# Kernel tuning notes

Measured on AMD Instinct MI355X. Metric: run time of the kernel, lower is better.

Reference implementation:

```python
import jax, jax.numpy as jnp
import numpy as np

TAU = 2.0        # LIF membrane time constant
VTH = 0.5        # spike threshold
EPS = 1e-5       # BatchNorm eps
ALPHA = 2.0      # ATan surrogate alpha (spikingjelly default)


@jax.custom_vjp
def atan_heaviside(x):
    # forward: Heaviside spike; backward: ATan surrogate gradient
    return (x >= 0.0).astype(x.dtype)

def _ah_fwd(x):
    return atan_heaviside(x), x

def _ah_bwd(x, g):
    return (g * (ALPHA / 2.0) / (1.0 + (jnp.pi / 2.0 * ALPHA * x) ** 2),)

atan_heaviside.defvjp(_ah_fwd, _ah_bwd)


def lif_multistep(x):
    # x: [T, ...] -> spikes [T, ...]; hard reset to 0, decay_input=True
    def step(v, xt):
        v = v + (xt - v) / TAU
        s = atan_heaviside(v - VTH)
        v = v * (1.0 - jax.lax.stop_gradient(s))  # detach_reset=True
        return v, s
    v0 = jnp.zeros_like(x[0])
    _, spikes = jax.lax.scan(step, v0, x)
    return spikes


def tape_pe(d_model, max_len, dtype):
    # tAPE (ConvTran): sinusoidal PE with d_model/max_len frequency scaling
    pos = jnp.arange(max_len, dtype=dtype)[:, None]
    div = jnp.exp(jnp.arange(0, d_model, 2, dtype=dtype) * (-np.log(10000.0) / d_model))
    arg = pos * div * (d_model / max_len)
    pe = jnp.zeros((max_len, d_model), dtype)
    pe = pe.at[:, 0::2].set(jnp.sin(arg))
    pe = pe.at[:, 1::2].set(jnp.cos(arg))
    return pe  # [N, D]


def setup_inputs() -> dict:
    key = jax.random.key(0)
    k1, k2 = jax.random.split(key)
    T, B, N, P, D = 4, 64, 196, 768, 256
    x = jax.random.normal(k1, (T, B, N, P), dtype=jnp.float32)
    W = jax.random.normal(k2, (D, P), dtype=jnp.float32) * 0.02
    gamma = jnp.ones((D,), dtype=jnp.float32)
    beta = jnp.zeros((D,), dtype=jnp.float32)
    return {"x": x, "W": W, "gamma": gamma, "beta": beta}


def reference(x, W, gamma, beta):
    T, B, N, P = x.shape
    D = W.shape[0]
    # patch linear (no bias): [T,B,N,P] @ [D,P]^T -> [T,B,N,D]
    h = jnp.einsum('tbnp,dp->tbnd', x, W)
    h = jnp.transpose(h, (0, 1, 3, 2))  # [T,B,D,N]
    # BatchNorm1d over channel D (training-mode batch stats over T*B and N)
    mean = h.mean(axis=(0, 1, 3), keepdims=True)
    var = ((h - mean) ** 2).mean(axis=(0, 1, 3), keepdims=True)
    h = (h - mean) * jax.lax.rsqrt(var + EPS)
    h = h * gamma[None, None, :, None] + beta[None, None, :, None]
    # LIF spiking neuron scan over T
    h = lif_multistep(h)
    # tAPE positional encoding (broadcast [D,N] over T,B) + second LIF
    h = h + tape_pe(D, N, h.dtype).T
    h = lif_multistep(h)
    return jnp.transpose(h, (0, 1, 3, 2))  # [T,B,N,D]
```

## Files before the change

kernel.cpp:

```cpp
#include <hip/hip_runtime.h>
#include <cmath>

#define T_    4
#define B_    64
#define N_    196
#define P_    768
#define D_    256
#define BN_   (B_*N_)
#define M_    (T_*BN_)
#define SITES (BN_*D_)

#define TILE  64
#define TK    16
#define MBLKS (M_/TILE)
#define NBLKS (D_/TILE)
#define LSTR  70

typedef __attribute__((ext_vector_type(2))) float f32x2;

extern "C" __global__ __launch_bounds__(256)
void gemm_f32emu(const float* __restrict__ x, const float* __restrict__ w,
                 float* __restrict__ h) {
#pragma clang fp contract(off)
    __shared__ __align__(16) f32x2 As2[TK/2][LSTR];
    __shared__ __align__(16) f32x2 Bs2[TK/2][LSTR];

    const int tid  = threadIdx.x;
    const int tx   = tid & 15;
    const int ty   = tid >> 4;
    const int bid  = blockIdx.x;
    const int xcd  = bid & 7;
    const int lin  = bid >> 3;
    const int m0   = (xcd * 98 + (lin >> 2)) * TILE;
    const int d0   = (lin & 3) * TILE;
    const int lrow = tid >> 2;
    const int kq   = tid & 3;
    const int lk   = kq * 4;
    const int srow  = lrow + 2 * ((lrow >> 4) & 3);
    const int abase = ty * 4 + 2 * ((ty >> 2) & 3);
    const int bbase = tx * 4 + 2 * ((tx >> 2) & 3);

    f32x2 acc[4][4][2];
#pragma unroll
    for (int i = 0; i < 4; ++i)
#pragma unroll
        for (int j = 0; j < 4; ++j)
#pragma unroll
            for (int p = 0; p < 2; ++p) acc[i][j][p] = f32x2{0.0f, 0.0f};

    for (int k0 = 0; k0 < P_; k0 += TK) {
        const float4 av = *(const float4*)(x + (size_t)(m0 + lrow) * P_ + k0 + lk);
        const float4 bv = *(const float4*)(w + (size_t)(d0 + lrow) * P_ + k0 + lk);
        As2[kq * 2 + 0][srow] = f32x2{av.x, av.y};
        As2[kq * 2 + 1][srow] = f32x2{av.z, av.w};
        Bs2[kq * 2 + 0][srow] = f32x2{bv.x, bv.y};
        Bs2[kq * 2 + 1][srow] = f32x2{bv.z, bv.w};
        __syncthreads();
#pragma unroll
        for (int kp = 0; kp < TK / 2; ++kp) {
            const int pi = kp & 1;
            const f32x2* Ar = As2[kp];
            const f32x2* Br = Bs2[kp];
            f32x2 a2[4], b2[4];
#pragma unroll
            for (int i = 0; i < 4; ++i) a2[i] = Ar[abase + i];
#pragma unroll
            for (int j = 0; j < 4; ++j) b2[j] = Br[bbase + j];
#pragma unroll
            for (int i = 0; i < 4; ++i)
#pragma unroll
                for (int j = 0; j < 4; ++j) {
                    const f32x2 p = a2[i] * b2[j];
                    acc[i][j][pi] = acc[i][j][pi] + p;
                }
        }
        __syncthreads();
    }

#pragma unroll
    for (int i = 0; i < 4; ++i) {
        float4 o;
        float* hv = &o.x;
#pragma unroll
        for (int j = 0; j < 4; ++j) {
            const float l01 = __fadd_rn(acc[i][j][0].x, acc[i][j][0].y);
            const float l23 = __fadd_rn(acc[i][j][1].x, acc[i][j][1].y);
            hv[j] = __fadd_rn(l01, l23);
        }
        *(float4*)(h + (size_t)(m0 + ty * 4 + i) * D_ + d0 + tx * 4) = o;
    }
}

extern "C" __global__ __launch_bounds__(256)
void transpose_hT(const float* __restrict__ h, float* __restrict__ hT) {
    __shared__ float tile[64][65];
    const int tid = threadIdx.x;
    const int m0 = blockIdx.x * 64;
    const int d0 = blockIdx.y * 64;
    const int r  = tid >> 4;
    const int c4 = (tid & 15) * 4;
#pragma unroll
    for (int i = 0; i < 4; ++i) {
        const float4 v = *(const float4*)&h[(size_t)(m0 + r + i * 16) * D_ + d0 + c4];
        *(float4*)&tile[r + i * 16][c4] = v;
    }
    __syncthreads();
#pragma unroll
    for (int i = 0; i < 4; ++i) {
        const int dr = r + i * 16;
        float4 o;
        o.x = tile[c4 + 0][dr];
        o.y = tile[c4 + 1][dr];
        o.z = tile[c4 + 2][dr];
        o.w = tile[c4 + 3][dr];
        *(float4*)&hT[(size_t)(d0 + dr) * M_ + m0 + c4] = o;
    }
}

#define MCH2 7168
extern "C" __global__ __launch_bounds__(256)
void mean_hT(const float* __restrict__ hT, float* __restrict__ mean_) {
    __shared__ float buf[2][MCH2];
    const int tid = threadIdx.x;
    const float* src = hT + (size_t)blockIdx.x * M_;

#pragma unroll
    for (int u = 0; u < 7; ++u)
        *(float4*)&buf[0][(u * 256 + tid) * 4] =
            *(const float4*)&src[(u * 256 + tid) * 4];
    __syncthreads();

    float acc = 0.0f;
    for (int c = 0; c < 7; ++c) {
        const int cb = c & 1;
        const bool have = (c + 1 < 7);
        float4 v[7];
        if (have) {
            const float* rp = src + (c + 1) * MCH2;
#pragma unroll
            for (int u = 0; u < 7; ++u)
                v[u] = *(const float4*)&rp[(u * 256 + tid) * 4];
        }
        if (tid == 0) {
            const float* bp = buf[cb];
#pragma unroll 16
            for (int m = 0; m < MCH2; ++m) acc = __fadd_rn(acc, bp[m]);
        }
        if (have) {
#pragma unroll
            for (int u = 0; u < 7; ++u)
                *(float4*)&buf[cb ^ 1][(u * 256 + tid) * 4] = v[u];
        }
        __syncthreads();
    }
    if (tid == 0) mean_[blockIdx.x] = __fdiv_rn(acc, 50176.0f);
}

extern "C" __global__ __launch_bounds__(256)
void var_hT(const float* __restrict__ hT, const float* __restrict__ mean_,
            float* __restrict__ inv_) {
    __shared__ float chunks[256];
    const int d    = blockIdx.x;
    const int tid  = threadIdx.x;
    const int wv   = tid >> 6;
    const int lane = tid & 63;
    const float mn = mean_[d];
    const float* col = hT + (size_t)d * M_;

    for (int tb = wv; tb < T_ * B_; tb += 4) {
        double part = 0.0;
        for (int n = lane; n < N_; n += 64) {
            const float hv = col[tb * N_ + n];
            const float t1 = __fsub_rn(hv, mn);
            const float sq = __fmul_rn(t1, t1);
            part += (double)sq;
        }
#pragma unroll
        for (int off = 32; off; off >>= 1) part += __shfl_down(part, off);
        if (lane == 0) chunks[tb] = (float)part;
    }
    __syncthreads();
    if (tid == 0) {
        float accf = 0.0f;
        for (int tb = 0; tb < T_ * B_; ++tb) accf = __fadd_rn(accf, chunks[tb]);
        const float var = __fdiv_rn(accf, 50176.0f);
        inv_[d] = __fdiv_rn(1.0f, __fsqrt_rn(__fadd_rn(var, 1e-5f)));
    }
}

#define MCH  256
#define DCH  16
#define PADW 20
#define NCHK (M_/MCH)

extern "C" __global__ __launch_bounds__(256)
void mean_seq(const float* __restrict__ h, float* __restrict__ mean_) {
    __shared__ __align__(16) float buf[2][MCH][PADW];
    const int tid = threadIdx.x;
    const int d0  = blockIdx.x * DCH;
    {
        const float* rp = h + (size_t)tid * D_ + d0;
        *(float4*)&buf[0][tid][0]  = *(const float4*)(rp + 0);
        *(float4*)&buf[0][tid][4]  = *(const float4*)(rp + 4);
        *(float4*)&buf[0][tid][8]  = *(const float4*)(rp + 8);
        *(float4*)&buf[0][tid][12] = *(const float4*)(rp + 12);
    }
    __syncthreads();
    float acc = 0.0f;
    for (int c = 0; c < NCHK; ++c) {
        const int cb = c & 1;
        const bool have = (c + 1 < NCHK);
        float4 v0, v1, v2, v3;
        if (have) {
            const float* rp = h + ((size_t)(c + 1) * MCH + tid) * D_ + d0;
            v0 = *(const float4*)(rp + 0);
            v1 = *(const float4*)(rp + 4);
            v2 = *(const float4*)(rp + 8);
            v3 = *(const float4*)(rp + 12);
        }
        if (tid < DCH) {
#pragma unroll 16
            for (int m = 0; m < MCH; ++m)
                acc = __fadd_rn(acc, buf[cb][m][tid]);
        }
        if (have) {
            *(float4*)&buf[cb ^ 1][tid][0]  = v0;
            *(float4*)&buf[cb ^ 1][tid][4]  = v1;
            *(float4*)&buf[cb ^ 1][tid][8]  = v2;
            *(float4*)&buf[cb ^ 1][tid][12] = v3;
        }
        __syncthreads();
    }
    if (tid < DCH) mean_[d0 + tid] = __fdiv_rn(acc, 50176.0f);
}

extern "C" __global__ __launch_bounds__(64)
void var_seq(const float* __restrict__ h, const float* __restrict__ mean_,
             float* __restrict__ inv_) {
    const int d    = blockIdx.x;
    const int lane = threadIdx.x;
    const float mn = mean_[d];
    float accf = 0.0f;
    for (int tb = 0; tb < T_ * B_; ++tb) {
        double part = 0.0;
        for (int n = lane; n < N_; n += 64) {
            const float hv = h[((size_t)tb * N_ + n) * D_ + d];
            const float t1 = __fsub_rn(hv, mn);
            const float sq = __fmul_rn(t1, t1);
            part += (double)sq;
        }
#pragma unroll
        for (int off = 32; off; off >>= 1) part += __shfl_down(part, off);
        accf = __fadd_rn(accf, (float)part);
    }
    if (lane == 0) {
        const float var = __fdiv_rn(accf, 50176.0f);
        inv_[d] = __fdiv_rn(1.0f, __fsqrt_rn(__fadd_rn(var, 1e-5f)));
    }
}

extern "C" __global__ __launch_bounds__(256)
void pe_build(float* __restrict__ pe_) {
    const int d = threadIdx.x;
    const int n = blockIdx.x;
    const double dv  = exp((double)(d & ~1) * (-9.210340371976184 / 256.0));
    const double arg = ((double)n * dv) * (256.0 / 196.0);
    pe_[(size_t)n * D_ + d] = (d & 1) ? (float)cos(arg) : (float)sin(arg);
}

extern "C" __global__ __launch_bounds__(256)
void lif_final(float* __restrict__ out, const float* __restrict__ mean_,
               const float* __restrict__ inv_, const float* __restrict__ gamma,
               const float* __restrict__ beta, const float* __restrict__ pe_tab) {
    const int idx = blockIdx.x * 256 + threadIdx.x;
    const int d = idx & (D_ - 1);
    const int n = (idx >> 8) % N_;

    const float mn = mean_[d];
    const float iv = inv_[d];
    const float g  = gamma[d];
    const float b  = beta[d];

    float pe;
    if (pe_tab) {
        pe = pe_tab[(size_t)n * D_ + d];
    } else {
        const double dv  = exp((double)(d & ~1) * (-9.210340371976184 / 256.0));
        const double arg = ((double)n * dv) * (256.0 / 196.0);
        pe = (d & 1) ? (float)cos(arg) : (float)sin(arg);
    }

    float hv[4];
#pragma unroll
    for (int t = 0; t < T_; ++t) hv[t] = out[(size_t)t * SITES + idx];

    float v1 = 0.0f, v2 = 0.0f, s2v[4];
#pragma unroll
    for (int t = 0; t < T_; ++t) {
        const float t1 = __fsub_rn(hv[t], mn);
        const float u  = __fmul_rn(t1, iv);
        const float hb = __fadd_rn(__fmul_rn(u, g), b);
        v1 = __fadd_rn(v1, __fmul_rn(__fsub_rn(hb, v1), 0.5f));
        const float s1 = (v1 >= 0.5f) ? 1.0f : 0.0f;
        v1 = __fmul_rn(v1, __fsub_rn(1.0f, s1));
        const float y = __fadd_rn(s1, pe);
        v2 = __fadd_rn(v2, __fmul_rn(__fsub_rn(y, v2), 0.5f));
        const float s2 = (v2 >= 0.5f) ? 1.0f : 0.0f;
        v2 = __fmul_rn(v2, __fsub_rn(1.0f, s2));
        s2v[t] = s2;
    }
#pragma unroll
    for (int t = 0; t < T_; ++t) out[(size_t)t * SITES + idx] = s2v[t];
}

extern "C" void kernel_launch(void* const* d_in, const int* in_sizes, int n_in,
                              void* d_out, int out_size, void* d_ws, size_t ws_size,
                              hipStream_t stream) {
    const float* x     = (const float*)d_in[0];
    const float* w     = (const float*)d_in[1];
    const float* gamma = (const float*)d_in[2];
    const float* beta  = (const float*)d_in[3];
    float* out = (float*)d_out;

    float* mean_ = (float*)d_ws;
    float* inv_  = mean_ + D_;
    float* pe_   = inv_  + D_;
    float* hT_   = pe_   + (size_t)N_ * D_;

    const size_t need_pe = (size_t)(2 * D_ + N_ * D_) * sizeof(float);
    const size_t need_hT = need_pe + (size_t)M_ * D_ * sizeof(float);
    const bool use_pe = ws_size >= need_pe;
    const bool use_hT = ws_size >= need_hT;

    gemm_f32emu<<<MBLKS * NBLKS, 256, 0, stream>>>(x, w, out);
    if (use_hT) {
        transpose_hT<<<dim3(MBLKS, NBLKS), 256, 0, stream>>>(out, hT_);
        mean_hT<<<D_, 256, 0, stream>>>(hT_, mean_);
        var_hT<<<D_, 256, 0, stream>>>(hT_, mean_, inv_);
    } else {
        mean_seq<<<16, 256, 0, stream>>>(out, mean_);
        var_seq<<<D_, 64, 0, stream>>>(out, mean_, inv_);
    }
    if (use_pe) pe_build<<<N_, 256, 0, stream>>>(pe_);
    lif_final<<<SITES / 256, 256, 0, stream>>>(out, mean_, inv_, gamma, beta,
                                               use_pe ? pe_ : nullptr);
}
```

Before: 957.8 us.

## Double-buffer GEMM LDS tiles, fuse transpose into GEMM epilogue, use packed asm

The GEMM now double-buffers its shared-memory tiles with one barrier per k-step, prefetching the next global tile during compute. Inline v_pk_mul/v_pk_add asm replaces the compiler's packed multiply-add so the rounding stays unfused. The GEMM epilogue also writes the transposed hT directly, which removes the separate transpose kernel and its extra pass over h. The serial mean reduction reads float2 values from LDS. The padding swizzle was dropped (LSTR 66), which may add LDS bank conflicts.

New measurement: 906.4 us. -5.4%, faster.

```diff
diff --git a/kernel.cpp b/kernel.cpp
--- a/kernel.cpp
+++ b/kernel.cpp
@@ -12,18 +12,25 @@
 
 #define TILE  64
 #define TK    16
+#define KITER (P_/TK)
 #define MBLKS (M_/TILE)
 #define NBLKS (D_/TILE)
-#define LSTR  70
+#define LSTR  66
 
 typedef __attribute__((ext_vector_type(2))) float f32x2;
 
+__device__ __forceinline__ void pk_fma(f32x2& acc, f32x2 a, f32x2 b) {
+    f32x2 t;
+    asm("v_pk_mul_f32 %1, %2, %3\n\t"
+        "v_pk_add_f32 %0, %0, %1"
+        : "+v"(acc), "=&v"(t) : "v"(a), "v"(b));
+}
+
 extern "C" __global__ __launch_bounds__(256)
 void gemm_f32emu(const float* __restrict__ x, const float* __restrict__ w,
-                 float* __restrict__ h) {
-#pragma clang fp contract(off)
-    __shared__ __align__(16) f32x2 As2[TK/2][LSTR];
-    __shared__ __align__(16) f32x2 Bs2[TK/2][LSTR];
+                 float* __restrict__ h, float* __restrict__ hT) {
+    __shared__ __align__(16) f32x2 As2[2][TK/2][LSTR];
+    __shared__ __align__(16) f32x2 Bs2[2][TK/2][LSTR];
 
     const int tid  = threadIdx.x;
     const int tx   = tid & 15;
@@ -36,9 +43,9 @@
     const int lrow = tid >> 2;
     const int kq   = tid & 3;
     const int lk   = kq * 4;
-    const int srow  = lrow + 2 * ((lrow >> 4) & 3);
-    const int abase = ty * 4 + 2 * ((ty >> 2) & 3);
-    const int bbase = tx * 4 + 2 * ((tx >> 2) & 3);
+
+    const float* xp = x + (size_t)(m0 + lrow) * P_ + lk;
+    const float* wp = w + (size_t)(d0 + lrow) * P_ + lk;
 
     f32x2 acc[4][4][2];
 #pragma unroll
@@ -48,72 +55,69 @@
 #pragma unroll
             for (int p = 0; p < 2; ++p) acc[i][j][p] = f32x2{0.0f, 0.0f};
 
-    for (int k0 = 0; k0 < P_; k0 += TK) {
-        const float4 av = *(const float4*)(x + (size_t)(m0 + lrow) * P_ + k0 + lk);
-        const float4 bv = *(const float4*)(w + (size_t)(d0 + lrow) * P_ + k0 + lk);
-        As2[kq * 2 + 0][srow] = f32x2{av.x, av.y};
-        As2[kq * 2 + 1][srow] = f32x2{av.z, av.w};
-        Bs2[kq * 2 + 0][srow] = f32x2{bv.x, bv.y};
-        Bs2[kq * 2 + 1][srow] = f32x2{bv.z, bv.w};
+    {
+        const float4 av = *(const float4*)xp;
+        const float4 bv = *(const float4*)wp;
+        As2[0][kq * 2 + 0][lrow] = f32x2{av.x, av.y};
+        As2[0][kq * 2 + 1][lrow] = f32x2{av.z, av.w};
+        Bs2[0][kq * 2 + 0][lrow] = f32x2{bv.x, bv.y};
+        Bs2[0][kq * 2 + 1][lrow] = f32x2{bv.z, bv.w};
+    }
+
+    int cur = 0;
+    for (int k0 = 0; k0 < KITER; ++k0) {
         __syncthreads();
+        float4 av, bv;
+        const bool have = (k0 + 1 < KITER);
+        if (have) {
+            av = *(const float4*)(xp + (k0 + 1) * TK);
+            bv = *(const float4*)(wp + (k0 + 1) * TK);
+        }
 #pragma unroll
         for (int kp = 0; kp < TK / 2; ++kp) {
             const int pi = kp & 1;
-            const f32x2* Ar = As2[kp];
-            const f32x2* Br = Bs2[kp];
+            const f32x2* Ar = As2[cur][kp];
+            const f32x2* Br = Bs2[cur][kp];
             f32x2 a2[4], b2[4];
 #pragma unroll
-            for (int i = 0; i < 4; ++i) a2[i] = Ar[abase + i];
-#pragma unroll
-            for (int j = 0; j < 4; ++j) b2[j] = Br[bbase + j];
+            for (int i = 0; i < 4; ++i) a2[i] = Ar[ty * 4 + i];
+#pragma unroll
+            for (int j = 0; j < 4; ++j) b2[j] = Br[tx * 4 + j];
 #pragma unroll
             for (int i = 0; i < 4; ++i)
 #pragma unroll
-                for (int j = 0; j < 4; ++j) {
-                    const f32x2 p = a2[i] * b2[j];
-                    acc[i][j][pi] = acc[i][j][pi] + p;
-                }
-        }
-        __syncthreads();
-    }
-
-#pragma unroll
-    for (int i = 0; i < 4; ++i) {
-        float4 o;
-        float* hv = &o.x;
+                for (int j = 0; j < 4; ++j)
+                    pk_fma(acc[i][j][pi], a2[i], b2[j]);
+        }
+        if (have) {
+            As2[cur ^ 1][kq * 2 + 0][lrow] = f32x2{av.x, av.y};
+            As2[cur ^ 1][kq * 2 + 1][lrow] = f32x2{av.z, av.w};
+            Bs2[cur ^ 1][kq * 2 + 0][lrow] = f32x2{bv.x, bv.y};
+            Bs2[cur ^ 1][kq * 2 + 1][lrow] = f32x2{bv.z, bv.w};
+        }
+        cur ^= 1;
+    }
+
+    float res[4][4];
+#pragma unroll
+    for (int i = 0; i < 4; ++i)
 #pragma unroll
         for (int j = 0; j < 4; ++j) {
             const float l01 = __fadd_rn(acc[i][j][0].x, acc[i][j][0].y);
             const float l23 = __fadd_rn(acc[i][j][1].x, acc[i][j][1].y);
-            hv[j] = __fadd_rn(l01, l23);
-        }
+            res[i][j] = __fadd_rn(l01, l23);
+        }
+#pragma unroll
+    for (int i = 0; i < 4; ++i) {
+        float4 o = {res[i][0], res[i][1], res[i][2], res[i][3]};
         *(float4*)(h + (size_t)(m0 + ty * 4 + i) * D_ + d0 + tx * 4) = o;
     }
-}
-
-extern "C" __global__ __launch_bounds__(256)
-void transpose_hT(const float* __restrict__ h, float* __restrict__ hT) {
-    __shared__ float tile[64][65];
-    const int tid = threadIdx.x;
-    const int m0 = blockIdx.x * 64;
-    const int d0 = blockIdx.y * 64;
-    const int r  = tid >> 4;
-    const int c4 = (tid & 15) * 4;
-#pragma unroll
-    for (int i = 0; i < 4; ++i) {
-        const float4 v = *(const float4*)&h[(size_t)(m0 + r + i * 16) * D_ + d0 + c4];
-        *(float4*)&tile[r + i * 16][c4] = v;
-    }
-    __syncthreads();
-#pragma unroll
-    for (int i = 0; i < 4; ++i) {
-        const int dr = r + i * 16;
-        float4 o;
-        o.x = tile[c4 + 0][dr];
-        o.y = tile[c4 + 1][dr];
-        o.z = tile[c4 + 2][dr];
-        o.w = tile[c4 + 3][dr];
-        *(float4*)&hT[(size_t)(d0 + dr) * M_ + m0 + c4] = o;
+    if (hT) {
+#pragma unroll
+        for (int j = 0; j < 4; ++j) {
+            float4 o = {res[0][j], res[1][j], res[2][j], res[3][j]};
+            *(float4*)(hT + (size_t)(d0 + tx * 4 + j) * M_ + m0 + ty * 4) = o;
+        }
     }
 }
 
@@ -142,9 +146,13 @@
                 v[u] = *(const float4*)&rp[(u * 256 + tid) * 4];
         }
         if (tid == 0) {
-            const float* bp = buf[cb];
-#pragma unroll 16
-            for (int m = 0; m < MCH2; ++m) acc = __fadd_rn(acc, bp[m]);
+            const float2* bp2 = (const float2*)buf[cb];
+#pragma unroll 8
+            for (int m2 = 0; m2 < MCH2 / 2; ++m2) {
+                const float2 vv = bp2[m2];
+                acc = __fadd_rn(acc, vv.x);
+                acc = __fadd_rn(acc, vv.y);
+            }
         }
         if (have) {
 #pragma unroll
@@ -332,9 +340,9 @@
     const bool use_pe = ws_size >= need_pe;
     const bool use_hT = ws_size >= need_hT;
 
-    gemm_f32emu<<<MBLKS * NBLKS, 256, 0, stream>>>(x, w, out);
+    gemm_f32emu<<<MBLKS * NBLKS, 256, 0, stream>>>(x, w, out,
+                                                   use_hT ? hT_ : nullptr);
     if (use_hT) {
-        transpose_hT<<<dim3(MBLKS, NBLKS), 256, 0, stream>>>(out, hT_);
         mean_hT<<<D_, 256, 0, stream>>>(hT_, mean_);
         var_hT<<<D_, 256, 0, stream>>>(hT_, mean_, inv_);
     } else {
```
